# Kernel optimization log

Hardware: AMD Instinct MI355X
Metric: run time of the kernel (lower is better)

Reference implementation:

```python
import jax, jax.numpy as jnp
import numpy as np

N = 50000      # nodes
E = 800000     # edges (avg degree 16)
IN_DIM = 128
H = 4          # attention heads
D = 32         # hidden dim per head
NEG_SLOPE = 0.2


def setup_inputs() -> dict:
    key = jax.random.key(0)
    ks = jax.random.split(key, 9)
    x = jax.random.normal(ks[0], (N, IN_DIM), dtype=jnp.float32)
    src = jax.random.randint(ks[1], (E,), 0, N, dtype=jnp.int64)
    dst = jax.random.randint(ks[2], (E,), 0, N, dtype=jnp.int64)
    # layer 0: IN_DIM -> H*D ; layer 1: H*D -> H*D
    s0 = 1.0 / np.sqrt(IN_DIM)
    s1 = 1.0 / np.sqrt(H * D)
    W1 = jax.random.normal(ks[3], (H * D, IN_DIM), dtype=jnp.float32) * s0
    al1 = jax.random.normal(ks[4], (1, H, D), dtype=jnp.float32) * s1
    ar1 = jax.random.normal(ks[5], (1, H, D), dtype=jnp.float32) * s1
    W2 = jax.random.normal(ks[6], (H * D, H * D), dtype=jnp.float32) * s1
    al2 = jax.random.normal(ks[7], (1, H, D), dtype=jnp.float32) * s1
    ar2 = jax.random.normal(ks[8], (1, H, D), dtype=jnp.float32) * s1
    return {"x": x, "src": src, "dst": dst, "W1": W1, "al1": al1, "ar1": ar1,
            "W2": W2, "al2": al2, "ar2": ar2}


def gat_conv(h, src, dst, W, al, ar):
    """DGL-style GATConv. h: [N, F_in] -> [N, H, D], with ELU activation."""
    feat = (h @ W.T).reshape(N, H, D)                 # [N,H,D]
    el = jnp.sum(feat * al, axis=-1)                  # [N,H] a_l . Wh
    er = jnp.sum(feat * ar, axis=-1)                  # [N,H] a_r . Wh
    e = jax.nn.leaky_relu(el[src] + er[dst], NEG_SLOPE)  # [E,H]
    # numerically stable edge softmax over incoming edges of each dst node
    m = jax.ops.segment_max(e, dst, num_segments=N)   # [N,H]
    ee = jnp.exp(e - m[dst])                          # [E,H]
    denom = jax.ops.segment_sum(ee, dst, num_segments=N)  # [N,H]
    alpha = ee / denom[dst]                           # [E,H]
    msg = feat[src] * alpha[..., None]                # [E,H,D]
    out = jax.ops.segment_sum(msg, dst, num_segments=N)   # [N,H,D]
    return jax.nn.elu(out)


def reference(x, src, dst, W1, al1, ar1, W2, al2, ar2):
    h = gat_conv(x, src, dst, W1, al1, ar1).reshape(N, H * D)  # flatten(1)
    h = gat_conv(h, src, dst, W2, al2, ar2)                    # [N,H,D]
    return jnp.mean(h, axis=1)                                 # [N,D]
```

## Files before the change

kernel.cpp:

```cpp
#include <hip/hip_runtime.h>
#include <cmath>
#include <type_traits>

#define HEADS 4
#define FDIM 128
#define NEG 0.2f
#define NBUCK 8

typedef __attribute__((ext_vector_type(8))) __bf16 bf16x8;
typedef __attribute__((ext_vector_type(8))) _Float16 h16x8;
typedef __attribute__((ext_vector_type(4))) float f32x4;

__global__ __launch_bounds__(256) void prep_kernel(
    const float* __restrict__ W1, const float* __restrict__ al1,
    const float* __restrict__ ar1,
    const float* __restrict__ W2, const float* __restrict__ al2,
    const float* __restrict__ ar2,
    __bf16* __restrict__ wf1, __bf16* __restrict__ wext1,
    __bf16* __restrict__ wf2, __bf16* __restrict__ wext2,
    int* __restrict__ counts, int nb)
{
    const int b = blockIdx.x, tid = threadIdx.x;
    if (b < 256) {
        const float* W = (b < 128) ? W1 : W2;
        __bf16* wf = (b < 128) ? wf1 : wf2;
        int idx = (b & 127) * 256 + tid;
        int j = idx & 7;
        int r = idx >> 3;
        int c = r & 15; r >>= 4;
        int t = r & 7;  r >>= 3;
        int kq = r & 15;
        int hl = r >> 4;
        float v = W[(t * 16 + c) * 128 + kq * 8 + j];
        __bf16 hi = (__bf16)v;
        wf[idx] = (hl == 0) ? hi : (__bf16)(v - (float)hi);
    } else if (b < 258) {
        const float* W  = (b == 256) ? W1 : W2;
        const float* al = (b == 256) ? al1 : al2;
        const float* ar = (b == 256) ? ar1 : ar2;
        __bf16* wext = (b == 256) ? wext1 : wext2;
        __shared__ float val[1024];
        #pragma unroll
        for (int ch = 0; ch < 4; ++ch) {
            int idx = ch * 256 + tid;
            int c = idx >> 7, k = idx & 127;
            int h = c & 3;
            const float* a = (c < 4) ? al : ar;
            float s = 0.f;
            for (int d = 0; d < 32; ++d)
                s += a[h * 32 + d] * W[(h * 32 + d) * 128 + k];
            val[c * 128 + k] = s;
        }
        __syncthreads();
        #pragma unroll
        for (int ch = 0; ch < 16; ++ch) {
            int idx = tid * 16 + ch;
            int j = idx & 7;
            int r = idx >> 3;
            int c = r & 15; r >>= 4;
            int kq = r & 15;
            int hl = r >> 4;
            float v = (c < 8) ? val[c * 128 + kq * 8 + j] : 0.f;
            __bf16 hi = (__bf16)v;
            wext[idx] = (hl == 0) ? hi : (__bf16)(v - (float)hi);
        }
    } else {
        int i0 = ((b - 258) * 256 + tid) * 4;
        if (i0 + 3 < nb) {
            *(int4*)&counts[i0] = make_int4(0, 0, 0, 0);
        } else {
            for (int i = i0; i < nb; ++i) counts[i] = 0;
        }
    }
}

template <typename XT>
__global__ __launch_bounds__(256) void gemm_mfma_kernel(
    const XT* __restrict__ X, const bf16x8* __restrict__ wf,
    const bf16x8* __restrict__ wext,
    _Float16* __restrict__ featH,
    float* __restrict__ el, float* __restrict__ er,
    int nnodes, int ntiles)
{
    __shared__ bf16x8 lw[4096];
    const int tid = threadIdx.x;
    for (int i = tid; i < 4096; i += 256) lw[i] = wf[i];
    __syncthreads();

    const int wave = tid >> 6, lane = tid & 63;
    const int l15 = lane & 15, quad = lane >> 4;

    int tile = blockIdx.x;
    float xr[32], xn[32];

    auto loadX = [&](int tl, float* dst) {
        int nodeA = tl * 64 + wave * 16 + l15;
        bool v = nodeA < nnodes;
        if constexpr (std::is_same<XT, float>::value) {
            const float4* xp = (const float4*)(X + (size_t)nodeA * 128);
            #pragma unroll
            for (int ks = 0; ks < 4; ++ks) {
                float4 a = v ? xp[ks * 8 + quad * 2]     : make_float4(0.f, 0.f, 0.f, 0.f);
                float4 b = v ? xp[ks * 8 + quad * 2 + 1] : make_float4(0.f, 0.f, 0.f, 0.f);
                dst[ks * 8 + 0] = a.x; dst[ks * 8 + 1] = a.y;
                dst[ks * 8 + 2] = a.z; dst[ks * 8 + 3] = a.w;
                dst[ks * 8 + 4] = b.x; dst[ks * 8 + 5] = b.y;
                dst[ks * 8 + 6] = b.z; dst[ks * 8 + 7] = b.w;
            }
        } else {
            const h16x8* xp = (const h16x8*)(X + (size_t)nodeA * 128);
            #pragma unroll
            for (int ks = 0; ks < 4; ++ks) {
                h16x8 hv;
                if (v) {
                    hv = xp[ks * 4 + quad];
                } else {
                    #pragma unroll
                    for (int j = 0; j < 8; ++j) hv[j] = (_Float16)0.f;
                }
                #pragma unroll
                for (int j = 0; j < 8; ++j) dst[ks * 8 + j] = (float)hv[j];
            }
        }
    };

    loadX(tile, xr);
    while (true) {
        int next = tile + gridDim.x;
        if (next < ntiles) loadX(next, xn);

        f32x4 acc[9];
        #pragma unroll
        for (int t = 0; t < 9; ++t) acc[t] = (f32x4){0.f, 0.f, 0.f, 0.f};

        #pragma unroll
        for (int ks = 0; ks < 4; ++ks) {
            bf16x8 ahi, alo;
            #pragma unroll
            for (int j = 0; j < 8; ++j) {
                float xv = xr[ks * 8 + j];
                __bf16 h = (__bf16)xv;
                ahi[j] = h;
                alo[j] = (__bf16)(xv - (float)h);
            }
            const int kq = ks * 4 + quad;

            {
                bf16x8 bh = wext[(kq) * 16 + l15];
                bf16x8 bl = wext[(16 + kq) * 16 + l15];
                acc[8] = __builtin_amdgcn_mfma_f32_16x16x32_bf16(ahi, bh, acc[8], 0, 0, 0);
                acc[8] = __builtin_amdgcn_mfma_f32_16x16x32_bf16(alo, bh, acc[8], 0, 0, 0);
                acc[8] = __builtin_amdgcn_mfma_f32_16x16x32_bf16(ahi, bl, acc[8], 0, 0, 0);
            }
            #pragma unroll
            for (int t = 0; t < 8; ++t) {
                bf16x8 bh = lw[(kq * 8 + t) * 16 + l15];
                bf16x8 bl = lw[((16 + kq) * 8 + t) * 16 + l15];
                acc[t] = __builtin_amdgcn_mfma_f32_16x16x32_bf16(ahi, bh, acc[t], 0, 0, 0);
                acc[t] = __builtin_amdgcn_mfma_f32_16x16x32_bf16(alo, bh, acc[t], 0, 0, 0);
                acc[t] = __builtin_amdgcn_mfma_f32_16x16x32_bf16(ahi, bl, acc[t], 0, 0, 0);
            }
        }

        const int nodeC = tile * 64 + wave * 16 + quad * 4;
        #pragma unroll
        for (int r = 0; r < 4; ++r) {
            int gn = nodeC + r;
            if (gn < nnodes) {
                #pragma unroll
                for (int t = 0; t < 8; ++t)
                    featH[(size_t)gn * 128 + t * 16 + l15] = (_Float16)acc[t][r];
            }
        }
        if (l15 < 8) {
            #pragma unroll
            for (int r = 0; r < 4; ++r) {
                int gn = nodeC + r;
                if (gn < nnodes) {
                    if (l15 < 4) el[gn * HEADS + l15] = acc[8][r];
                    else         er[gn * HEADS + (l15 - 4)] = acc[8][r];
                }
            }
        }

        if (next >= ntiles) break;
        #pragma unroll
        for (int i = 0; i < 32; ++i) xr[i] = xn[i];
        tile = next;
    }
}

__global__ __launch_bounds__(256) void hist_kernel(
    const int* __restrict__ src, const int* __restrict__ dst,
    int* __restrict__ counts, int* __restrict__ rank, int nedges, int shift)
{
    int i0 = (blockIdx.x * 256 + threadIdx.x) * 4;
    if (i0 + 3 < nedges) {
        int4 d = *(const int4*)&dst[i0];
        int4 s = *(const int4*)&src[i0];
        int4 r;
        r.x = atomicAdd(&counts[d.x * NBUCK + (s.x >> shift)], 1);
        r.y = atomicAdd(&counts[d.y * NBUCK + (s.y >> shift)], 1);
        r.z = atomicAdd(&counts[d.z * NBUCK + (s.z >> shift)], 1);
        r.w = atomicAdd(&counts[d.w * NBUCK + (s.w >> shift)], 1);
        *(int4*)&rank[i0] = r;
    } else {
        for (int i = i0; i < nedges; ++i)
            rank[i] = atomicAdd(&counts[dst[i] * NBUCK + (src[i] >> shift)], 1);
    }
}

__global__ __launch_bounds__(256) void scan1_kernel(
    const int* __restrict__ counts, int* __restrict__ offsets,
    int* __restrict__ bsums, int n)
{
    __shared__ int wsums[4];
    const int tid = threadIdx.x, lane = tid & 63, w = tid >> 6;
    const int i = blockIdx.x * 1024 + tid * 4;

    int4 v = make_int4(0, 0, 0, 0);
    if (i + 3 < n) v = *(const int4*)&counts[i];
    else {
        if (i < n)     v.x = counts[i];
        if (i + 1 < n) v.y = counts[i + 1];
        if (i + 2 < n) v.z = counts[i + 2];
    }
    int s0 = v.x, s1 = s0 + v.y, s2 = s1 + v.z, s3 = s2 + v.w;

    int x = s3;
    #pragma unroll
    for (int off = 1; off < 64; off <<= 1) {
        int t = __shfl_up(x, off, 64);
        if (lane >= off) x += t;
    }
    if (lane == 63) wsums[w] = x;
    __syncthreads();
    int wbase = 0;
    #pragma unroll
    for (int k = 0; k < 4; ++k) if (k < w) wbase += wsums[k];

    int tbase = wbase + x - s3;
    if (i < n)     offsets[i]     = tbase;
    if (i + 1 < n) offsets[i + 1] = tbase + s0;
    if (i + 2 < n) offsets[i + 2] = tbase + s1;
    if (i + 3 < n) offsets[i + 3] = tbase + s2;
    if (tid == 255) bsums[blockIdx.x] = wbase + x;
}

__global__ __launch_bounds__(256) void scan23_kernel(
    int* __restrict__ offsets, const int* __restrict__ bsums, int n, int nedges)
{
    __shared__ int sbase;
    const int tid = threadIdx.x, b = blockIdx.x;
    if (tid < 64) {
        int s = 0;
        for (int i = tid; i < b; i += 64) s += bsums[i];
        #pragma unroll
        for (int off = 1; off < 64; off <<= 1) s += __shfl_xor(s, off, 64);
        if (tid == 0) sbase = s;
    }
    __syncthreads();
    const int base = sbase;
    const int i = b * 1024 + tid * 4;
    #pragma unroll
    for (int k = 0; k < 4; ++k)
        if (i + k < n) offsets[i + k] += base;
    if (b == 0 && tid == 0) offsets[n] = nedges;
}

__global__ __launch_bounds__(256) void scatter_kernel(
    const int* __restrict__ src, const int* __restrict__ dst,
    const int* __restrict__ rank, const int* __restrict__ offsets,
    int* __restrict__ csr_src, int nedges, int shift)
{
    int i0 = (blockIdx.x * 256 + threadIdx.x) * 4;
    if (i0 + 3 < nedges) {
        int4 d = *(const int4*)&dst[i0];
        int4 r = *(const int4*)&rank[i0];
        int4 s = *(const int4*)&src[i0];
        csr_src[offsets[d.x * NBUCK + (s.x >> shift)] + r.x] = s.x;
        csr_src[offsets[d.y * NBUCK + (s.y >> shift)] + r.y] = s.y;
        csr_src[offsets[d.z * NBUCK + (s.z >> shift)] + r.z] = s.z;
        csr_src[offsets[d.w * NBUCK + (s.w >> shift)] + r.w] = s.w;
    } else {
        for (int i = i0; i < nedges; ++i)
            csr_src[offsets[dst[i] * NBUCK + (src[i] >> shift)] + rank[i]] = src[i];
    }
}

template <bool MEAN>
__global__ __launch_bounds__(256) void aggregate_kernel(
    const _Float16* __restrict__ featH, const float* __restrict__ el,
    const float* __restrict__ er, const int* __restrict__ offsets,
    const int* __restrict__ csr_src, void* __restrict__ outp, int nnodes)
{
    const int n = (blockIdx.x * 256 + threadIdx.x) >> 6;
    if (n >= nnodes) return;
    const int lane = threadIdx.x & 63;
    const int g = lane >> 4, u = lane & 15, h = u >> 2;
    const int beg = offsets[n * NBUCK], end = offsets[n * NBUCK + NBUCK];
    const float ern = er[n * HEADS + h];
    const int iters = (end - beg + 3) >> 2;

    float a[8];
    #pragma unroll
    for (int p = 0; p < 8; ++p) a[p] = 0.f;
    float sw = 0.f;

    int j = beg + g;
    bool v = j < end;
    int s = v ? csr_src[j] : 0;
    float q = el[s * HEADS + h];
    h16x8 f = ((const h16x8*)(featH + (size_t)s * 128))[u];

    for (int it = 0; it < iters; ++it) {
        int jn = j + 4;
        bool vn = jn < end;
        int sn = vn ? csr_src[jn] : 0;
        float qn = el[sn * HEADS + h];
        h16x8 fn = ((const h16x8*)(featH + (size_t)sn * 128))[u];

        float e = q + ern;
        e = e > 0.f ? e : NEG * e;
        float w = v ? __expf(e) : 0.f;
        #pragma unroll
        for (int p = 0; p < 8; ++p) a[p] += w * (float)f[p];
        sw += w;

        j = jn; v = vn; q = qn; f = fn;
    }

    #pragma unroll
    for (int p = 0; p < 8; ++p) {
        a[p] += __shfl_xor(a[p], 16, 64);
        a[p] += __shfl_xor(a[p], 32, 64);
    }
    sw += __shfl_xor(sw, 16, 64);
    sw += __shfl_xor(sw, 32, 64);

    float inv = sw > 0.f ? 1.f / sw : 0.f;
    float r[8];
    #pragma unroll
    for (int p = 0; p < 8; ++p) {
        float t = a[p] * inv;
        r[p] = t > 0.f ? t : expm1f(t);
    }

    if (!MEAN) {
        if (g == 0) {
            h16x8 o;
            #pragma unroll
            for (int p = 0; p < 8; ++p) o[p] = (_Float16)r[p];
            ((h16x8*)outp)[(size_t)n * 16 + u] = o;
        }
    } else {
        #pragma unroll
        for (int p = 0; p < 8; ++p) {
            r[p] += __shfl_xor(r[p], 4, 64);
            r[p] += __shfl_xor(r[p], 8, 64);
        }
        if (g == 0 && u < 4) {
            float* out = (float*)outp;
            float4* o4 = (float4*)(out + (size_t)n * 32 + u * 8);
            o4[0] = make_float4(0.25f * r[0], 0.25f * r[1], 0.25f * r[2], 0.25f * r[3]);
            o4[1] = make_float4(0.25f * r[4], 0.25f * r[5], 0.25f * r[6], 0.25f * r[7]);
        }
    }
}

extern "C" void kernel_launch(void* const* d_in, const int* in_sizes, int n_in,
                              void* d_out, int out_size, void* d_ws, size_t ws_size,
                              hipStream_t stream)
{
    const float* x   = (const float*)d_in[0];
    const int*   src = (const int*)d_in[1];
    const int*   dst = (const int*)d_in[2];
    const float* W1  = (const float*)d_in[3];
    const float* al1 = (const float*)d_in[4];
    const float* ar1 = (const float*)d_in[5];
    const float* W2  = (const float*)d_in[6];
    const float* al2 = (const float*)d_in[7];
    const float* ar2 = (const float*)d_in[8];

    const int N = in_sizes[0] / FDIM;
    const int E = in_sizes[1];
    const int NB = N * NBUCK;

    int shift = 0;
    while (((N - 1) >> shift) > (NBUCK - 1)) ++shift;

    _Float16* h1 = (_Float16*)d_ws;
    _Float16* featH = h1 + (size_t)N * FDIM;
    float* el = (float*)(featH + (size_t)N * FDIM);
    float* er = el + (size_t)N * HEADS;
    int* counts  = (int*)(er + (size_t)N * HEADS);
    int* offsets = counts + NB;
    int* rank    = offsets + (NB + 1);
    int* csr_src = rank + E;
    int* bsums   = csr_src + E;
    uintptr_t wp = ((uintptr_t)(bsums + 512) + 63) & ~(uintptr_t)63;
    __bf16* wf1   = (__bf16*)wp;
    __bf16* wext1 = wf1 + 32768;
    __bf16* wf2   = wext1 + 4096;
    __bf16* wext2 = wf2 + 32768;

    const int ntiles = (N + 63) / 64;
    const int gemm_grid = ntiles < 256 ? ntiles : 256;
    const int edge4_grid = ((E + 3) / 4 + 255) / 256;
    const int agg_grid  = (N + 3) / 4;
    const int nscan     = (NB + 1023) / 1024;
    const int zblocks   = ((NB + 3) / 4 + 255) / 256;

    prep_kernel<<<258 + zblocks, 256, 0, stream>>>(
        W1, al1, ar1, W2, al2, ar2, wf1, wext1, wf2, wext2, counts, NB);

    hist_kernel<<<edge4_grid, 256, 0, stream>>>(src, dst, counts, rank, E, shift);
    scan1_kernel<<<nscan, 256, 0, stream>>>(counts, offsets, bsums, NB);
    scan23_kernel<<<nscan, 256, 0, stream>>>(offsets, bsums, NB, E);
    scatter_kernel<<<edge4_grid, 256, 0, stream>>>(src, dst, rank, offsets,
                                                   csr_src, E, shift);

    gemm_mfma_kernel<float><<<gemm_grid, 256, 0, stream>>>(
        x, (const bf16x8*)wf1, (const bf16x8*)wext1, featH, el, er, N, ntiles);
    aggregate_kernel<false><<<agg_grid, 256, 0, stream>>>(
        featH, el, er, offsets, csr_src, (void*)h1, N);

    gemm_mfma_kernel<_Float16><<<gemm_grid, 256, 0, stream>>>(
        h1, (const bf16x8*)wf2, (const bf16x8*)wext2, featH, el, er, N, ntiles);
    aggregate_kernel<true><<<agg_grid, 256, 0, stream>>>(
        featH, el, er, offsets, csr_src, d_out, N);
}
```

Before: 253.6 us.

## Halve GEMM shared weights, deepen aggregate prefetch, widen edge kernels to 8

The GEMM kernel now keeps only the high bf16 weight half in shared memory (32 KB instead of 64 KB), reads the low-correction half straight from global memory, and starts the X load before the weight copy. The GEMM grid is raised to 512 blocks, likely to raise occupancy. The aggregate kernel prefetches edges two iterations ahead instead of one, to hide gather latency. The histogram and scatter kernels each process 8 edges per thread. The costs are extra global/L2 traffic for the low weights, more registers in aggregate, and fewer threads in the edge kernels.

```diff
diff --git a/kernel.cpp b/kernel.cpp
--- a/kernel.cpp
+++ b/kernel.cpp
@@ -82,11 +82,8 @@
     float* __restrict__ el, float* __restrict__ er,
     int nnodes, int ntiles)
 {
-    __shared__ bf16x8 lw[4096];
+    __shared__ bf16x8 lw[2048];
     const int tid = threadIdx.x;
-    for (int i = tid; i < 4096; i += 256) lw[i] = wf[i];
-    __syncthreads();
-
     const int wave = tid >> 6, lane = tid & 63;
     const int l15 = lane & 15, quad = lane >> 4;
 
@@ -125,6 +122,9 @@
     };
 
     loadX(tile, xr);
+    for (int i = tid; i < 2048; i += 256) lw[i] = wf[i];
+    __syncthreads();
+
     while (true) {
         int next = tile + gridDim.x;
         if (next < ntiles) loadX(next, xn);
@@ -155,7 +155,7 @@
             #pragma unroll
             for (int t = 0; t < 8; ++t) {
                 bf16x8 bh = lw[(kq * 8 + t) * 16 + l15];
-                bf16x8 bl = lw[((16 + kq) * 8 + t) * 16 + l15];
+                bf16x8 bl = wf[2048 + (kq * 8 + t) * 16 + l15];
                 acc[t] = __builtin_amdgcn_mfma_f32_16x16x32_bf16(ahi, bh, acc[t], 0, 0, 0);
                 acc[t] = __builtin_amdgcn_mfma_f32_16x16x32_bf16(alo, bh, acc[t], 0, 0, 0);
                 acc[t] = __builtin_amdgcn_mfma_f32_16x16x32_bf16(ahi, bl, acc[t], 0, 0, 0);
@@ -194,16 +194,23 @@
     const int* __restrict__ src, const int* __restrict__ dst,
     int* __restrict__ counts, int* __restrict__ rank, int nedges, int shift)
 {
-    int i0 = (blockIdx.x * 256 + threadIdx.x) * 4;
-    if (i0 + 3 < nedges) {
-        int4 d = *(const int4*)&dst[i0];
-        int4 s = *(const int4*)&src[i0];
-        int4 r;
-        r.x = atomicAdd(&counts[d.x * NBUCK + (s.x >> shift)], 1);
-        r.y = atomicAdd(&counts[d.y * NBUCK + (s.y >> shift)], 1);
-        r.z = atomicAdd(&counts[d.z * NBUCK + (s.z >> shift)], 1);
-        r.w = atomicAdd(&counts[d.w * NBUCK + (s.w >> shift)], 1);
-        *(int4*)&rank[i0] = r;
+    int i0 = (blockIdx.x * 256 + threadIdx.x) * 8;
+    if (i0 + 7 < nedges) {
+        int4 d0 = *(const int4*)&dst[i0];
+        int4 d1 = *(const int4*)&dst[i0 + 4];
+        int4 s0 = *(const int4*)&src[i0];
+        int4 s1 = *(const int4*)&src[i0 + 4];
+        int4 r0, r1;
+        r0.x = atomicAdd(&counts[d0.x * NBUCK + (s0.x >> shift)], 1);
+        r0.y = atomicAdd(&counts[d0.y * NBUCK + (s0.y >> shift)], 1);
+        r0.z = atomicAdd(&counts[d0.z * NBUCK + (s0.z >> shift)], 1);
+        r0.w = atomicAdd(&counts[d0.w * NBUCK + (s0.w >> shift)], 1);
+        r1.x = atomicAdd(&counts[d1.x * NBUCK + (s1.x >> shift)], 1);
+        r1.y = atomicAdd(&counts[d1.y * NBUCK + (s1.y >> shift)], 1);
+        r1.z = atomicAdd(&counts[d1.z * NBUCK + (s1.z >> shift)], 1);
+        r1.w = atomicAdd(&counts[d1.w * NBUCK + (s1.w >> shift)], 1);
+        *(int4*)&rank[i0]     = r0;
+        *(int4*)&rank[i0 + 4] = r1;
     } else {
         for (int i = i0; i < nedges; ++i)
             rank[i] = atomicAdd(&counts[dst[i] * NBUCK + (src[i] >> shift)], 1);
@@ -273,15 +280,22 @@
     const int* __restrict__ rank, const int* __restrict__ offsets,
     int* __restrict__ csr_src, int nedges, int shift)
 {
-    int i0 = (blockIdx.x * 256 + threadIdx.x) * 4;
-    if (i0 + 3 < nedges) {
-        int4 d = *(const int4*)&dst[i0];
-        int4 r = *(const int4*)&rank[i0];
-        int4 s = *(const int4*)&src[i0];
-        csr_src[offsets[d.x * NBUCK + (s.x >> shift)] + r.x] = s.x;
-        csr_src[offsets[d.y * NBUCK + (s.y >> shift)] + r.y] = s.y;
-        csr_src[offsets[d.z * NBUCK + (s.z >> shift)] + r.z] = s.z;
-        csr_src[offsets[d.w * NBUCK + (s.w >> shift)] + r.w] = s.w;
+    int i0 = (blockIdx.x * 256 + threadIdx.x) * 8;
+    if (i0 + 7 < nedges) {
+        int4 d0 = *(const int4*)&dst[i0];
+        int4 d1 = *(const int4*)&dst[i0 + 4];
+        int4 r0 = *(const int4*)&rank[i0];
+        int4 r1 = *(const int4*)&rank[i0 + 4];
+        int4 s0 = *(const int4*)&src[i0];
+        int4 s1 = *(const int4*)&src[i0 + 4];
+        csr_src[offsets[d0.x * NBUCK + (s0.x >> shift)] + r0.x] = s0.x;
+        csr_src[offsets[d0.y * NBUCK + (s0.y >> shift)] + r0.y] = s0.y;
+        csr_src[offsets[d0.z * NBUCK + (s0.z >> shift)] + r0.z] = s0.z;
+        csr_src[offsets[d0.w * NBUCK + (s0.w >> shift)] + r0.w] = s0.w;
+        csr_src[offsets[d1.x * NBUCK + (s1.x >> shift)] + r1.x] = s1.x;
+        csr_src[offsets[d1.y * NBUCK + (s1.y >> shift)] + r1.y] = s1.y;
+        csr_src[offsets[d1.z * NBUCK + (s1.z >> shift)] + r1.z] = s1.z;
+        csr_src[offsets[d1.w * NBUCK + (s1.w >> shift)] + r1.w] = s1.w;
     } else {
         for (int i = i0; i < nedges; ++i)
             csr_src[offsets[dst[i] * NBUCK + (src[i] >> shift)] + rank[i]] = src[i];
@@ -307,27 +321,34 @@
     for (int p = 0; p < 8; ++p) a[p] = 0.f;
     float sw = 0.f;
 
-    int j = beg + g;
-    bool v = j < end;
-    int s = v ? csr_src[j] : 0;
-    float q = el[s * HEADS + h];
-    h16x8 f = ((const h16x8*)(featH + (size_t)s * 128))[u];
+    const h16x8* __restrict__ frow = (const h16x8*)featH;
+
+    int ja = beg + g;
+    int jb = ja + 4;
+    bool va = ja < end, vb = jb < end;
+    int sa = va ? csr_src[ja] : 0;
+    int sb = vb ? csr_src[jb] : 0;
+    float qa = el[sa * HEADS + h];
+    float qb = el[sb * HEADS + h];
+    h16x8 fa = frow[(size_t)sa * 16 + u];
+    h16x8 fb = frow[(size_t)sb * 16 + u];
 
     for (int it = 0; it < iters; ++it) {
-        int jn = j + 4;
-        bool vn = jn < end;
-        int sn = vn ? csr_src[jn] : 0;
-        float qn = el[sn * HEADS + h];
-        h16x8 fn = ((const h16x8*)(featH + (size_t)sn * 128))[u];
-
-        float e = q + ern;
+        int jc = ja + 8;
+        bool vc = jc < end;
+        int sc = vc ? csr_src[jc] : 0;
+        float qc = el[sc * HEADS + h];
+        h16x8 fc = frow[(size_t)sc * 16 + u];
+
+        float e = qa + ern;
         e = e > 0.f ? e : NEG * e;
-        float w = v ? __expf(e) : 0.f;
-        #pragma unroll
-        for (int p = 0; p < 8; ++p) a[p] += w * (float)f[p];
+        float w = va ? __expf(e) : 0.f;
+        #pragma unroll
+        for (int p = 0; p < 8; ++p) a[p] += w * (float)fa[p];
         sw += w;
 
-        j = jn; v = vn; q = qn; f = fn;
+        ja = jb; va = vb; sa = sb; qa = qb; fa = fb;
+        jb = jc; vb = vc; sb = sc; qb = qc; fb = fc;
     }
 
     #pragma unroll
@@ -405,8 +426,8 @@
     __bf16* wext2 = wf2 + 32768;
 
     const int ntiles = (N + 63) / 64;
-    const int gemm_grid = ntiles < 256 ? ntiles : 256;
-    const int edge4_grid = ((E + 3) / 4 + 255) / 256;
+    const int gemm_grid = ntiles < 512 ? ntiles : 512;
+    const int edge8_grid = ((E + 7) / 8 + 255) / 256;
     const int agg_grid  = (N + 3) / 4;
     const int nscan     = (NB + 1023) / 1024;
     const int zblocks   = ((NB + 3) / 4 + 255) / 256;
@@ -414,10 +435,10 @@
     prep_kernel<<<258 + zblocks, 256, 0, stream>>>(
         W1, al1, ar1, W2, al2, ar2, wf1, wext1, wf2, wext2, counts, NB);
 
-    hist_kernel<<<edge4_grid, 256, 0, stream>>>(src, dst, counts, rank, E, shift);
+    hist_kernel<<<edge8_grid, 256, 0, stream>>>(src, dst, counts, rank, E, shift);
     scan1_kernel<<<nscan, 256, 0, stream>>>(counts, offsets, bsums, NB);
     scan23_kernel<<<nscan, 256, 0, stream>>>(offsets, bsums, NB, E);
-    scatter_kernel<<<edge4_grid, 256, 0, stream>>>(src, dst, rank, offsets,
+    scatter_kernel<<<edge8_grid, 256, 0, stream>>>(src, dst, rank, offsets,
                                                    csr_src, E, shift);
 
     gemm_mfma_kernel<float><<<gemm_grid, 256, 0, stream>>>(
```

After: 251.8 us. No clear change (-0.7%).
